# Kernel optimization log

Measured on AMD Instinct MI355X. Metric: run time of the kernel, lower is better.

The kernel has to match this reference:

```python
import jax, jax.numpy as jnp
import numpy as np

N, E = 50000, 1600000
D_IN, D_HID, D_OUT = 256, 256, 128  # 2*output_dim = 256, output_dim = 128


def glorot(key, shape):
    fan_in, fan_out = shape
    limit = np.sqrt(6.0 / (fan_in + fan_out)).astype(np.float32)
    return jax.random.uniform(key, shape, jnp.float32, -limit, limit)


def setup_inputs() -> dict:
    key = jax.random.key(0)
    k0, k1, k2, k3 = jax.random.split(key, 4)
    x = jax.random.normal(k0, (N, D_IN), jnp.float32)
    edge_index = jax.random.randint(k1, (2, E), 0, N, jnp.int32)
    W1 = glorot(k2, (D_IN, D_HID))
    b1 = jnp.zeros((D_HID,), jnp.float32)
    W2 = glorot(k3, (D_HID, D_OUT))
    b2 = jnp.zeros((D_OUT,), jnp.float32)
    return {"x": x, "edge_index": edge_index, "W1": W1, "b1": b1, "W2": W2, "b2": b2}


def gcn_propagate(x, src, dst, num_nodes):
    """One hop of D^-1/2 (A + I) D^-1/2 @ x (PyG gcn_norm with self-loops)."""
    loops = jnp.arange(num_nodes, dtype=src.dtype)
    src_sl = jnp.concatenate([src, loops])  # [E + N]
    dst_sl = jnp.concatenate([dst, loops])
    ones = jnp.ones(src_sl.shape, x.dtype)
    deg = jax.ops.segment_sum(ones, dst_sl, num_segments=num_nodes)  # >= 1 (self-loop)
    dinv = jax.lax.rsqrt(jnp.maximum(deg, 1e-12))
    norm = dinv[src_sl] * dinv[dst_sl]  # [E + N]
    msgs = x[src_sl] * norm[:, None]    # gather + scale, [E+N, D]
    return jax.ops.segment_sum(msgs, dst_sl, num_segments=num_nodes)


def reference(x, edge_index, W1, b1, W2, b2):
    src, dst = edge_index[0], edge_index[1]
    n = x.shape[0]
    # SGConv(K=1): propagate then linear. conv1 + ReLU
    h = jax.nn.relu(gcn_propagate(x, src, dst, n) @ W1 + b1)
    # conv2 (GAE branch)
    return gcn_propagate(h, src, dst, n) @ W2 + b2
```

## Files before the change

### kernel.cpp

```cpp
#include <hip/hip_runtime.h>

typedef short s16x8 __attribute__((ext_vector_type(8)));
typedef float f32x4 __attribute__((ext_vector_type(4)));
typedef float f32x2 __attribute__((ext_vector_type(2)));

#define TILE 2048

__device__ __forceinline__ unsigned int brne(float f) {
    unsigned int u = __float_as_uint(f);
    return (u + 0x7FFFu + ((u >> 16) & 1u)) >> 16;
}
__device__ __forceinline__ float blo(unsigned int u) { return __uint_as_float(u << 16); }
__device__ __forceinline__ float bhi(unsigned int u) { return __uint_as_float(u & 0xFFFF0000u); }

__device__ __forceinline__ void acc8(float* a, const uint4 u, const float wt) {
    a[0] += blo(u.x) * wt; a[1] += bhi(u.x) * wt;
    a[2] += blo(u.y) * wt; a[3] += bhi(u.y) * wt;
    a[4] += blo(u.z) * wt; a[5] += bhi(u.z) * wt;
    a[6] += blo(u.w) * wt; a[7] += bhi(u.w) * wt;
}

__device__ __forceinline__ unsigned int enc_fp8(float v) {
    return __builtin_amdgcn_cvt_pk_fp8_f32(v, v, 0, false) & 0xFF;
}
__device__ __forceinline__ void acc16p(f32x2* a, const uint4 u, const f32x2 w2) {
    a[0] += __builtin_amdgcn_cvt_pk_f32_fp8((int)u.x, false) * w2;
    a[1] += __builtin_amdgcn_cvt_pk_f32_fp8((int)u.x, true)  * w2;
    a[2] += __builtin_amdgcn_cvt_pk_f32_fp8((int)u.y, false) * w2;
    a[3] += __builtin_amdgcn_cvt_pk_f32_fp8((int)u.y, true)  * w2;
    a[4] += __builtin_amdgcn_cvt_pk_f32_fp8((int)u.z, false) * w2;
    a[5] += __builtin_amdgcn_cvt_pk_f32_fp8((int)u.z, true)  * w2;
    a[6] += __builtin_amdgcn_cvt_pk_f32_fp8((int)u.w, false) * w2;
    a[7] += __builtin_amdgcn_cvt_pk_f32_fp8((int)u.w, true)  * w2;
}


__global__ void k_bhist(const int* __restrict__ dst, int* __restrict__ bucket_cnt,
                        int e, int nb) {
    __shared__ int h[256];
    const int tid = threadIdx.x;
    h[tid] = 0;
    __syncthreads();
    const int base = blockIdx.x * TILE + tid;
#pragma unroll
    for (int k = 0; k < 8; k++) {
        const int i = base + k * 256;
        if (i < e) atomicAdd(&h[dst[i] >> 8], 1);
    }
    __syncthreads();
    if (tid < nb && h[tid]) atomicAdd(&bucket_cnt[tid], h[tid]);
}

__global__ void k_bscan(const int* __restrict__ bucket_cnt, int* __restrict__ bucket_base,
                        int* __restrict__ bucket_cursor, int nb, int e) {
    __shared__ int sh[256];
    const int tid = threadIdx.x;
    const int v = (tid < nb) ? bucket_cnt[tid] : 0;
    int x = v;
    sh[tid] = x;
    __syncthreads();
    for (int off = 1; off < 256; off <<= 1) {
        const int t = (tid >= off) ? sh[tid - off] : 0;
        __syncthreads();
        if (tid >= off) { x += t; sh[tid] = x; }
        __syncthreads();
    }
    if (tid < nb) { bucket_base[tid] = x - v; bucket_cursor[tid] = x - v; }
    if (tid == 0) bucket_base[nb] = e;
}

__global__ void k_bscatter(const int* __restrict__ src, const int* __restrict__ dst,
                           int* __restrict__ bucket_cursor, uint2* __restrict__ eb, int e) {
    __shared__ int h[256], hbase[256], h2[256];
    const int tid = threadIdx.x;
    h[tid] = 0; h2[tid] = 0;
    __syncthreads();
    const int base = blockIdx.x * TILE + tid;
    int s[8], d[8], b[8];
    bool val[8];
#pragma unroll
    for (int k = 0; k < 8; k++) {
        const int i = base + k * 256;
        val[k] = i < e;
        if (val[k]) {
            s[k] = src[i]; d[k] = dst[i]; b[k] = d[k] >> 8;
            atomicAdd(&h[b[k]], 1);
        }
    }
    __syncthreads();
    if (h[tid]) hbase[tid] = atomicAdd(&bucket_cursor[tid], h[tid]);
    __syncthreads();
#pragma unroll
    for (int k = 0; k < 8; k++) {
        if (val[k]) {
            const int off = atomicAdd(&h2[b[k]], 1);
            eb[hbase[b[k]] + off] = make_uint2((unsigned)s[k], (unsigned)d[k]);
        }
    }
}

__global__ void k_nhist_scan(const uint2* __restrict__ eb, const int* __restrict__ bucket_base,
                             int* __restrict__ rowptr, int* __restrict__ part,
                             float* __restrict__ dinv, int n) {
    __shared__ int c[256], sh[256];
    const int tid = threadIdx.x, b = blockIdx.x;
    c[tid] = 0;
    __syncthreads();
    const int beg = bucket_base[b], end = bucket_base[b + 1];
    for (int i = beg + tid; i < end; i += 256)
        atomicAdd(&c[eb[i].y & 255], 1);
    __syncthreads();
    const int v = c[tid];
    const int node = b * 256 + tid;
    if (node < n) dinv[node] = rsqrtf((float)(v + 1));
    int x = v;
    sh[tid] = x;
    __syncthreads();
    for (int off = 1; off < 256; off <<= 1) {
        const int t = (tid >= off) ? sh[tid - off] : 0;
        __syncthreads();
        if (tid >= off) { x += t; sh[tid] = x; }
        __syncthreads();
    }
    if (node <= n) rowptr[node] = x - v;
    if (tid == 255) part[b] = x;
}

__global__ void k_place(const uint2* __restrict__ eb, const int* __restrict__ bucket_base,
                        int* __restrict__ rowptr, const int* __restrict__ part,
                        int* __restrict__ es, int n, int nb) {
    __shared__ int sh[256], rp[256], offs[256];
    const int tid = threadIdx.x, b = blockIdx.x;
    int x = (tid < nb) ? part[tid] : 0;
    sh[tid] = x;
    __syncthreads();
    for (int off = 1; off < 256; off <<= 1) {
        const int t = (tid >= off) ? sh[tid - off] : 0;
        __syncthreads();
        if (tid >= off) { x += t; sh[tid] = x; }
        __syncthreads();
    }
    const int prefix = (b > 0) ? sh[b - 1] : 0;
    const int node = b * 256 + tid;
    int rg = 0;
    if (node <= n) {
        rg = rowptr[node] + prefix;
        rowptr[node] = rg;
    }
    rp[tid] = rg;
    offs[tid] = 0;
    __syncthreads();
    const int beg = bucket_base[b], end = bucket_base[b + 1];
    for (int i = beg + tid; i < end; i += 256) {
        const uint2 ed = eb[i];
        const int d = (int)ed.y & 255;
        const int local = atomicAdd(&offs[d], 1);
        es[rp[d] + local] = (int)ed.x;
    }
}

__global__ void k_tW2(const float* __restrict__ W1, const float* __restrict__ W2,
                      unsigned short* __restrict__ W1t, unsigned short* __restrict__ W2t) {
    const int t = blockIdx.x * 256 + threadIdx.x;
    if (t < 65536) {
        const int k = t >> 8, nn = t & 255;
        W1t[nn * 256 + k] = (unsigned short)brne(W1[t]);
    } else {
        const int u = t - 65536;
        const int k = u >> 7, nn = u & 127;
        W2t[nn * 256 + k] = (unsigned short)brne(W2[u]);
    }
}

#define LP 40
template <bool AF32, bool FP8OUT>
__global__ __launch_bounds__(256) void k_gemm(const void* __restrict__ Av,
                                              const unsigned short* __restrict__ Bt,
                                              void* __restrict__ Cout,
                                              int M, int Nc) {
    __shared__ unsigned short As[128 * LP];
    __shared__ unsigned short Bs[128 * LP];

    const int tid = threadIdx.x;
    const int wave = tid >> 6, lane = tid & 63;
    const int wm = (wave >> 1) * 64, wn = (wave & 1) * 64;
    const int l15 = lane & 15, quad = lane >> 4;
    const int mBase = blockIdx.x * 128, nBase = blockIdx.y * 128;

    f32x4 acc[4][4];
#pragma unroll
    for (int i = 0; i < 4; i++)
#pragma unroll
        for (int j = 0; j < 4; j++) acc[i][j] = (f32x4){0.f, 0.f, 0.f, 0.f};

    const int r0 = tid >> 2, kc0 = tid & 3;
    int am0 = mBase + r0;      if (am0 >= M) am0 = M - 1;
    int am1 = mBase + r0 + 64; if (am1 >= M) am1 = M - 1;

    const uint4* Ap0; const uint4* Ap1; const float4* Af0; const float4* Af1;
    if (AF32) {
        Af0 = (const float4*)Av + (size_t)am0 * 64 + kc0 * 2;
        Af1 = (const float4*)Av + (size_t)am1 * 64 + kc0 * 2;
    } else {
        Ap0 = (const uint4*)Av + (size_t)am0 * 32 + kc0;
        Ap1 = (const uint4*)Av + (size_t)am1 * 32 + kc0;
    }
    const uint4* Bp0 = (const uint4*)Bt + (size_t)(nBase + r0) * 32 + kc0;
    const uint4* Bp1 = (const uint4*)Bt + (size_t)(nBase + r0 + 64) * 32 + kc0;

    for (int kt = 0; kt < 8; ++kt) {
        uint4 a0, a1;
        if (AF32) {
            const float4 l0 = Af0[kt * 8], h0 = Af0[kt * 8 + 1];
            const float4 l1 = Af1[kt * 8], h1 = Af1[kt * 8 + 1];
            a0.x = brne(l0.x) | (brne(l0.y) << 16); a0.y = brne(l0.z) | (brne(l0.w) << 16);
            a0.z = brne(h0.x) | (brne(h0.y) << 16); a0.w = brne(h0.z) | (brne(h0.w) << 16);
            a1.x = brne(l1.x) | (brne(l1.y) << 16); a1.y = brne(l1.z) | (brne(l1.w) << 16);
            a1.z = brne(h1.x) | (brne(h1.y) << 16); a1.w = brne(h1.z) | (brne(h1.w) << 16);
        } else {
            a0 = Ap0[kt * 4];
            a1 = Ap1[kt * 4];
        }
        const uint4 b0 = Bp0[kt * 4];
        const uint4 b1 = Bp1[kt * 4];
        __syncthreads();
        *(uint4*)&As[r0 * LP + kc0 * 8] = a0;
        *(uint4*)&As[(r0 + 64) * LP + kc0 * 8] = a1;
        *(uint4*)&Bs[r0 * LP + kc0 * 8] = b0;
        *(uint4*)&Bs[(r0 + 64) * LP + kc0 * 8] = b1;
        __syncthreads();

        s16x8 af[4], bf[4];
#pragma unroll
        for (int i = 0; i < 4; i++)
            af[i] = *(const s16x8*)&As[(wm + i * 16 + l15) * LP + quad * 8];
#pragma unroll
        for (int j = 0; j < 4; j++)
            bf[j] = *(const s16x8*)&Bs[(wn + j * 16 + l15) * LP + quad * 8];
#pragma unroll
        for (int i = 0; i < 4; i++)
#pragma unroll
            for (int j = 0; j < 4; j++)
                acc[i][j] = __builtin_amdgcn_mfma_f32_16x16x32_bf16(af[i], bf[j], acc[i][j], 0, 0, 0);
    }

#pragma unroll
    for (int i = 0; i < 4; i++) {
        const int rowb = mBase + wm + i * 16 + quad * 4;
#pragma unroll
        for (int r = 0; r < 4; r++) {
            const int row = rowb + r;
            if (row < M) {
#pragma unroll
                for (int j = 0; j < 4; j++) {
                    const int col = nBase + wn + j * 16 + l15;
                    if (FP8OUT)
                        ((unsigned char*)Cout)[(size_t)row * Nc + col] =
                            (unsigned char)enc_fp8(acc[i][j][r]);
                    else
                        ((unsigned short*)Cout)[(size_t)row * Nc + col] =
                            (unsigned short)brne(acc[i][j][r]);
                }
            }
        }
    }
}

__global__ void k_prop256f8(const uint4* __restrict__ X4,
                            const int* __restrict__ rowptr,
                            const int* __restrict__ es,
                            const float* __restrict__ dinv,
                            const float* __restrict__ bias,
                            uint4* __restrict__ Y4, int n) {
    const int wid = (int)((blockIdx.x * blockDim.x + threadIdx.x) >> 6);
    const int lane = threadIdx.x & 63;
    const int quad = lane >> 4, l16 = lane & 15;
    if (wid >= n) return;
    const float dd = dinv[wid];
    f32x2 a[8];
#pragma unroll
    for (int k = 0; k < 8; k++) a[k] = (f32x2){0.f, 0.f};

    const int beg = rowptr[wid], end = rowptr[wid + 1];
    int j = beg + quad;
    int sc0 = 0, sc1 = 0;
    float wc0 = 0.f, wc1 = 0.f;
    if (j < end)     { sc0 = es[j];     wc0 = dinv[sc0] * dd; }
    if (j + 4 < end) { sc1 = es[j + 4]; wc1 = dinv[sc1] * dd; }
    if (quad == 0) {
        const uint4 v = X4[(size_t)wid * 16 + l16];
        acc16p(a, v, (f32x2){dd * dd, dd * dd});
    }
    for (; j + 4 < end; j += 8) {
        const uint4 u0 = X4[(size_t)sc0 * 16 + l16];
        const uint4 u1 = X4[(size_t)sc1 * 16 + l16];
        const int jn0 = j + 8, jn1 = j + 12;
        const int sn0 = es[jn0 < end ? jn0 : end - 1];
        const int sn1 = es[jn1 < end ? jn1 : end - 1];
        const float wn0 = dinv[sn0] * dd, wn1 = dinv[sn1] * dd;
        acc16p(a, u0, (f32x2){wc0, wc0});
        acc16p(a, u1, (f32x2){wc1, wc1});
        sc0 = sn0; sc1 = sn1; wc0 = wn0; wc1 = wn1;
    }
    if (j < end) {
        const uint4 u0 = X4[(size_t)sc0 * 16 + l16];
        acc16p(a, u0, (f32x2){wc0, wc0});
    }
#pragma unroll
    for (int k = 0; k < 8; k++) {
        a[k][0] += __shfl_xor(a[k][0], 16);
        a[k][1] += __shfl_xor(a[k][1], 16);
        a[k][0] += __shfl_xor(a[k][0], 32);
        a[k][1] += __shfl_xor(a[k][1], 32);
    }
    if (quad == 0) {
        const float4* bp = (const float4*)bias + l16 * 4;
#pragma unroll
        for (int q = 0; q < 4; q++) {
            const float4 b = bp[q];
            a[2 * q][0]     = fmaxf(a[2 * q][0] + b.x, 0.f);
            a[2 * q][1]     = fmaxf(a[2 * q][1] + b.y, 0.f);
            a[2 * q + 1][0] = fmaxf(a[2 * q + 1][0] + b.z, 0.f);
            a[2 * q + 1][1] = fmaxf(a[2 * q + 1][1] + b.w, 0.f);
        }
        uint4 p0, p1;
        p0.x = brne(a[0][0]) | (brne(a[0][1]) << 16);
        p0.y = brne(a[1][0]) | (brne(a[1][1]) << 16);
        p0.z = brne(a[2][0]) | (brne(a[2][1]) << 16);
        p0.w = brne(a[3][0]) | (brne(a[3][1]) << 16);
        p1.x = brne(a[4][0]) | (brne(a[4][1]) << 16);
        p1.y = brne(a[5][0]) | (brne(a[5][1]) << 16);
        p1.z = brne(a[6][0]) | (brne(a[6][1]) << 16);
        p1.w = brne(a[7][0]) | (brne(a[7][1]) << 16);
        Y4[(size_t)wid * 32 + l16 * 2] = p0;
        Y4[(size_t)wid * 32 + l16 * 2 + 1] = p1;
    }
}

__global__ void k_prop128b(const uint4* __restrict__ X4,
                           const int* __restrict__ rowptr,
                           const int* __restrict__ es,
                           const float* __restrict__ dinv,
                           const float* __restrict__ bias,
                           float* __restrict__ Yout, int n) {
    const int wid = (int)((blockIdx.x * blockDim.x + threadIdx.x) >> 6);
    const int lane = threadIdx.x & 63;
    const int quad = lane >> 4, l16 = lane & 15;
    if (wid >= n) return;
    const float dd = dinv[wid];
    float a[8];
#pragma unroll
    for (int k = 0; k < 8; k++) a[k] = 0.f;

    const int beg = rowptr[wid], end = rowptr[wid + 1];
    int j = beg + quad;
    int sc0 = 0, sc1 = 0;
    float wc0 = 0.f, wc1 = 0.f;
    if (j < end)     { sc0 = es[j];     wc0 = dinv[sc0] * dd; }
    if (j + 4 < end) { sc1 = es[j + 4]; wc1 = dinv[sc1] * dd; }
    if (quad == 0) {
        const uint4 v = X4[(size_t)wid * 16 + l16];
        acc8(a, v, dd * dd);
    }
    for (; j + 4 < end; j += 8) {
        const uint4 u0 = X4[(size_t)sc0 * 16 + l16];
        const uint4 u1 = X4[(size_t)sc1 * 16 + l16];
        const int jn0 = j + 8, jn1 = j + 12;
        const int sn0 = es[jn0 < end ? jn0 : end - 1];
        const int sn1 = es[jn1 < end ? jn1 : end - 1];
        const float wn0 = dinv[sn0] * dd, wn1 = dinv[sn1] * dd;
        acc8(a, u0, wc0);
        acc8(a, u1, wc1);
        sc0 = sn0; sc1 = sn1; wc0 = wn0; wc1 = wn1;
    }
    if (j < end) {
        const uint4 u0 = X4[(size_t)sc0 * 16 + l16];
        acc8(a, u0, wc0);
    }
#pragma unroll
    for (int k = 0; k < 8; k++) {
        a[k] += __shfl_xor(a[k], 16);
        a[k] += __shfl_xor(a[k], 32);
    }
    if (quad == 0) {
        const float4 b0 = ((const float4*)bias)[l16 * 2];
        const float4 b1 = ((const float4*)bias)[l16 * 2 + 1];
        float4* op = (float4*)Yout + (size_t)wid * 32 + l16 * 2;
        op[0] = make_float4(a[0] + b0.x, a[1] + b0.y, a[2] + b0.z, a[3] + b0.w);
        op[1] = make_float4(a[4] + b1.x, a[5] + b1.y, a[6] + b1.z, a[7] + b1.w);
    }
}

extern "C" void kernel_launch(void* const* d_in, const int* in_sizes, int n_in,
                              void* d_out, int out_size, void* d_ws, size_t ws_size,
                              hipStream_t stream) {
    const float* x  = (const float*)d_in[0];
    const int*   ei = (const int*)d_in[1];
    const float* W1 = (const float*)d_in[2];
    const float* b1 = (const float*)d_in[3];
    const float* W2 = (const float*)d_in[4];
    const float* b2 = (const float*)d_in[5];
    float* out = (float*)d_out;

    const int n = in_sizes[0] / 256;
    const int e = in_sizes[1] / 2;
    const int* src = ei;
    const int* dst = ei + e;
    const int nb = (n + 255) >> 8;

    char* wsp = (char*)d_ws;
    size_t off = 0;
    auto alloc = [&](size_t bytes) -> char* {
        char* p = wsp + off;
        off += (bytes + 511) & ~(size_t)511;
        return p;
    };
    float* dinv    = (float*)alloc(sizeof(float) * n);
    int*   rowptr  = (int*)alloc(sizeof(int) * (n + 1));
    int*   part    = (int*)alloc(sizeof(int) * 256);
    int*   bcnt    = (int*)alloc(sizeof(int) * 256);
    int*   bbase   = (int*)alloc(sizeof(int) * 257);
    int*   bcur    = (int*)alloc(sizeof(int) * 256);
    int*   es      = (int*)alloc(sizeof(int) * e);
    unsigned short* W1t = (unsigned short*)alloc(2ull * 256 * 256);
    unsigned short* W2t = (unsigned short*)alloc(2ull * 128 * 256);
    unsigned char*  T1  = (unsigned char*)alloc((size_t)n * 256);
    unsigned short* H   = (unsigned short*)alloc(2ull * n * 256);
    unsigned short* T2  = (unsigned short*)alloc(2ull * n * 128);
    uint2* eb = (uint2*)H;

    const int nb_t = (e + TILE - 1) / TILE;

    (void)hipMemsetAsync(bcnt, 0, sizeof(int) * 256, stream);
    k_bhist<<<nb_t, 256, 0, stream>>>(dst, bcnt, e, nb);
    k_bscan<<<1, 256, 0, stream>>>(bcnt, bbase, bcur, nb, e);
    k_bscatter<<<nb_t, 256, 0, stream>>>(src, dst, bcur, eb, e);
    k_nhist_scan<<<nb, 256, 0, stream>>>(eb, bbase, rowptr, part, dinv, n);
    k_place<<<nb, 256, 0, stream>>>(eb, bbase, rowptr, part, es, n, nb);

    k_tW2<<<(65536 + 32768) / 256, 256, 0, stream>>>(W1, W2, W1t, W2t);

    dim3 g1((n + 127) / 128, 2);
    k_gemm<true, true><<<g1, 256, 0, stream>>>(x, W1t, T1, n, 256);
    k_prop256f8<<<(n + 3) / 4, 256, 0, stream>>>((const uint4*)T1, rowptr, es,
                                                 dinv, b1, (uint4*)H, n);

    dim3 g2((n + 127) / 128, 1);
    k_gemm<false, false><<<g2, 256, 0, stream>>>(H, W2t, T2, n, 128);
    k_prop128b<<<(n + 3) / 4, 256, 0, stream>>>((const uint4*)T2, rowptr, es,
                                                dinv, b2, out, n);
}
```

Baseline: 320.7 us.

## Precompute edge weights in CSR, fuse weight transpose, deepen gather pipeline, packed converts

Several changes land together. The CSR placement kernel can now store (src, weight) pairs with the per-edge normalisation precomputed, so the propagation kernels no longer do a dependent dinv gather per edge. The propagation loops now keep four edges in flight instead of two, using predicated zero-weight tail edges. Separately, the weight transpose is folded into the histogram launch, and bf16/fp8 conversions use packed hardware convert instructions, including paired row stores in the GEMM epilogue. Storing 8-byte edge records doubles the edge-list traffic, and the paired-weight path is only taken when the workspace is large enough.

```diff
diff --git a/kernel.cpp b/kernel.cpp
--- a/kernel.cpp
+++ b/kernel.cpp
@@ -13,16 +13,19 @@
 __device__ __forceinline__ float blo(unsigned int u) { return __uint_as_float(u << 16); }
 __device__ __forceinline__ float bhi(unsigned int u) { return __uint_as_float(u & 0xFFFF0000u); }
 
-__device__ __forceinline__ void acc8(float* a, const uint4 u, const float wt) {
-    a[0] += blo(u.x) * wt; a[1] += bhi(u.x) * wt;
-    a[2] += blo(u.y) * wt; a[3] += bhi(u.y) * wt;
-    a[4] += blo(u.z) * wt; a[5] += bhi(u.z) * wt;
-    a[6] += blo(u.w) * wt; a[7] += bhi(u.w) * wt;
-}
-
-__device__ __forceinline__ unsigned int enc_fp8(float v) {
-    return __builtin_amdgcn_cvt_pk_fp8_f32(v, v, 0, false) & 0xFF;
-}
+__device__ __forceinline__ unsigned int pk_bf16(float lo, float hi) {
+    unsigned int r;
+    asm("v_cvt_pk_bf16_f32 %0, %1, %2" : "=v"(r) : "v"(lo), "v"(hi));
+    return r;
+}
+
+__device__ __forceinline__ void acc8p(f32x2* a, const uint4 u, const f32x2 w2) {
+    a[0] += (f32x2){blo(u.x), bhi(u.x)} * w2;
+    a[1] += (f32x2){blo(u.y), bhi(u.y)} * w2;
+    a[2] += (f32x2){blo(u.z), bhi(u.z)} * w2;
+    a[3] += (f32x2){blo(u.w), bhi(u.w)} * w2;
+}
+
 __device__ __forceinline__ void acc16p(f32x2* a, const uint4 u, const f32x2 w2) {
     a[0] += __builtin_amdgcn_cvt_pk_f32_fp8((int)u.x, false) * w2;
     a[1] += __builtin_amdgcn_cvt_pk_f32_fp8((int)u.x, true)  * w2;
@@ -35,10 +38,24 @@
 }
 
 
-__global__ void k_bhist(const int* __restrict__ dst, int* __restrict__ bucket_cnt,
-                        int e, int nb) {
+__global__ void k_bhist_tw(const int* __restrict__ dst, int* __restrict__ bucket_cnt,
+                           int e, int nb, int nbt,
+                           const float* __restrict__ W1, const float* __restrict__ W2,
+                           unsigned short* __restrict__ W1t, unsigned short* __restrict__ W2t) {
+    const int tid = threadIdx.x;
+    if ((int)blockIdx.x >= nbt) {
+        const int t = ((int)blockIdx.x - nbt) * 256 + tid;
+        if (t < 65536) {
+            const int k = t >> 8, nn = t & 255;
+            W1t[nn * 256 + k] = (unsigned short)brne(W1[t]);
+        } else {
+            const int u = t - 65536;
+            const int k = u >> 7, nn = u & 127;
+            W2t[nn * 256 + k] = (unsigned short)brne(W2[u]);
+        }
+        return;
+    }
     __shared__ int h[256];
-    const int tid = threadIdx.x;
     h[tid] = 0;
     __syncthreads();
     const int base = blockIdx.x * TILE + tid;
@@ -126,10 +143,13 @@
     if (tid == 255) part[b] = x;
 }
 
+template <bool PREW>
 __global__ void k_place(const uint2* __restrict__ eb, const int* __restrict__ bucket_base,
                         int* __restrict__ rowptr, const int* __restrict__ part,
-                        int* __restrict__ es, int n, int nb) {
+                        void* __restrict__ esv, const float* __restrict__ dinv,
+                        int n, int nb) {
     __shared__ int sh[256], rp[256], offs[256];
+    __shared__ float sdv[256];
     const int tid = threadIdx.x, b = blockIdx.x;
     int x = (tid < nb) ? part[tid] : 0;
     sh[tid] = x;
@@ -149,26 +169,26 @@
     }
     rp[tid] = rg;
     offs[tid] = 0;
+    if (PREW) sdv[tid] = (node < n) ? dinv[node] : 0.f;
     __syncthreads();
     const int beg = bucket_base[b], end = bucket_base[b + 1];
-    for (int i = beg + tid; i < end; i += 256) {
-        const uint2 ed = eb[i];
-        const int d = (int)ed.y & 255;
-        const int local = atomicAdd(&offs[d], 1);
-        es[rp[d] + local] = (int)ed.x;
-    }
-}
-
-__global__ void k_tW2(const float* __restrict__ W1, const float* __restrict__ W2,
-                      unsigned short* __restrict__ W1t, unsigned short* __restrict__ W2t) {
-    const int t = blockIdx.x * 256 + threadIdx.x;
-    if (t < 65536) {
-        const int k = t >> 8, nn = t & 255;
-        W1t[nn * 256 + k] = (unsigned short)brne(W1[t]);
+    if (PREW) {
+        int2* es2 = (int2*)esv;
+        for (int i = beg + tid; i < end; i += 256) {
+            const uint2 ed = eb[i];
+            const int sI = (int)ed.x, d = (int)ed.y & 255;
+            const float w = dinv[sI] * sdv[d];
+            const int local = atomicAdd(&offs[d], 1);
+            es2[rp[d] + local] = make_int2(sI, __float_as_int(w));
+        }
     } else {
-        const int u = t - 65536;
-        const int k = u >> 7, nn = u & 127;
-        W2t[nn * 256 + k] = (unsigned short)brne(W2[u]);
+        int* es1 = (int*)esv;
+        for (int i = beg + tid; i < end; i += 256) {
+            const uint2 ed = eb[i];
+            const int d = (int)ed.y & 255;
+            const int local = atomicAdd(&offs[d], 1);
+            es1[rp[d] + local] = (int)ed.x;
+        }
     }
 }
 
@@ -213,10 +233,10 @@
         if (AF32) {
             const float4 l0 = Af0[kt * 8], h0 = Af0[kt * 8 + 1];
             const float4 l1 = Af1[kt * 8], h1 = Af1[kt * 8 + 1];
-            a0.x = brne(l0.x) | (brne(l0.y) << 16); a0.y = brne(l0.z) | (brne(l0.w) << 16);
-            a0.z = brne(h0.x) | (brne(h0.y) << 16); a0.w = brne(h0.z) | (brne(h0.w) << 16);
-            a1.x = brne(l1.x) | (brne(l1.y) << 16); a1.y = brne(l1.z) | (brne(l1.w) << 16);
-            a1.z = brne(h1.x) | (brne(h1.y) << 16); a1.w = brne(h1.z) | (brne(h1.w) << 16);
+            a0.x = pk_bf16(l0.x, l0.y); a0.y = pk_bf16(l0.z, l0.w);
+            a0.z = pk_bf16(h0.x, h0.y); a0.w = pk_bf16(h0.z, h0.w);
+            a1.x = pk_bf16(l1.x, l1.y); a1.y = pk_bf16(l1.z, l1.w);
+            a1.z = pk_bf16(h1.x, h1.y); a1.w = pk_bf16(h1.z, h1.w);
         } else {
             a0 = Ap0[kt * 4];
             a1 = Ap1[kt * 4];
@@ -248,27 +268,38 @@
     for (int i = 0; i < 4; i++) {
         const int rowb = mBase + wm + i * 16 + quad * 4;
 #pragma unroll
-        for (int r = 0; r < 4; r++) {
-            const int row = rowb + r;
-            if (row < M) {
-#pragma unroll
-                for (int j = 0; j < 4; j++) {
-                    const int col = nBase + wn + j * 16 + l15;
-                    if (FP8OUT)
-                        ((unsigned char*)Cout)[(size_t)row * Nc + col] =
-                            (unsigned char)enc_fp8(acc[i][j][r]);
-                    else
-                        ((unsigned short*)Cout)[(size_t)row * Nc + col] =
-                            (unsigned short)brne(acc[i][j][r]);
+        for (int j = 0; j < 4; j++) {
+            const int col = nBase + wn + j * 16 + l15;
+#pragma unroll
+            for (int r = 0; r < 4; r += 2) {
+                if (FP8OUT) {
+                    const unsigned int pk = __builtin_amdgcn_cvt_pk_fp8_f32(
+                        acc[i][j][r], acc[i][j][r + 1], 0, false);
+                    if (rowb + r < M)
+                        ((unsigned char*)Cout)[(size_t)(rowb + r) * Nc + col] =
+                            (unsigned char)pk;
+                    if (rowb + r + 1 < M)
+                        ((unsigned char*)Cout)[(size_t)(rowb + r + 1) * Nc + col] =
+                            (unsigned char)(pk >> 8);
+                } else {
+                    const unsigned int pk = pk_bf16(acc[i][j][r], acc[i][j][r + 1]);
+                    if (rowb + r < M)
+                        ((unsigned short*)Cout)[(size_t)(rowb + r) * Nc + col] =
+                            (unsigned short)pk;
+                    if (rowb + r + 1 < M)
+                        ((unsigned short*)Cout)[(size_t)(rowb + r + 1) * Nc + col] =
+                            (unsigned short)(pk >> 16);
                 }
             }
         }
     }
 }
 
+
+template <bool PREW>
 __global__ void k_prop256f8(const uint4* __restrict__ X4,
                             const int* __restrict__ rowptr,
-                            const int* __restrict__ es,
+                            const void* __restrict__ esv,
                             const float* __restrict__ dinv,
                             const float* __restrict__ bias,
                             uint4* __restrict__ Y4, int n) {
@@ -277,34 +308,60 @@
     const int quad = lane >> 4, l16 = lane & 15;
     if (wid >= n) return;
     const float dd = dinv[wid];
+    const int2* es2 = (const int2*)esv;
+    const int*  es1 = (const int*)esv;
     f32x2 a[8];
 #pragma unroll
     for (int k = 0; k < 8; k++) a[k] = (f32x2){0.f, 0.f};
 
     const int beg = rowptr[wid], end = rowptr[wid + 1];
     int j = beg + quad;
-    int sc0 = 0, sc1 = 0;
-    float wc0 = 0.f, wc1 = 0.f;
-    if (j < end)     { sc0 = es[j];     wc0 = dinv[sc0] * dd; }
-    if (j + 4 < end) { sc1 = es[j + 4]; wc1 = dinv[sc1] * dd; }
+
+    auto EDGE = [&](int jj, int& s, float& w) {
+        const bool v = jj < end;
+        const int idx = v ? jj : 0;
+        if (PREW) {
+            const int2 p = es2[idx];
+            s = p.x;
+            w = v ? __int_as_float(p.y) : 0.f;
+        } else {
+            s = es1[idx];
+            w = v ? dinv[s] * dd : 0.f;
+        }
+    };
+
+    int s0, s1, s2, s3;
+    float w0, w1, w2, w3;
+    EDGE(j, s0, w0); EDGE(j + 4, s1, w1); EDGE(j + 8, s2, w2); EDGE(j + 12, s3, w3);
+
     if (quad == 0) {
         const uint4 v = X4[(size_t)wid * 16 + l16];
         acc16p(a, v, (f32x2){dd * dd, dd * dd});
     }
-    for (; j + 4 < end; j += 8) {
-        const uint4 u0 = X4[(size_t)sc0 * 16 + l16];
-        const uint4 u1 = X4[(size_t)sc1 * 16 + l16];
-        const int jn0 = j + 8, jn1 = j + 12;
-        const int sn0 = es[jn0 < end ? jn0 : end - 1];
-        const int sn1 = es[jn1 < end ? jn1 : end - 1];
-        const float wn0 = dinv[sn0] * dd, wn1 = dinv[sn1] * dd;
-        acc16p(a, u0, (f32x2){wc0, wc0});
-        acc16p(a, u1, (f32x2){wc1, wc1});
-        sc0 = sn0; sc1 = sn1; wc0 = wn0; wc1 = wn1;
-    }
-    if (j < end) {
-        const uint4 u0 = X4[(size_t)sc0 * 16 + l16];
-        acc16p(a, u0, (f32x2){wc0, wc0});
+
+    while (j + 12 < end) {
+        const uint4 u0 = X4[(size_t)s0 * 16 + l16];
+        const uint4 u1 = X4[(size_t)s1 * 16 + l16];
+        const uint4 u2 = X4[(size_t)s2 * 16 + l16];
+        const uint4 u3 = X4[(size_t)s3 * 16 + l16];
+        j += 16;
+        int t0, t1, t2, t3;
+        float x0, x1, x2, x3;
+        EDGE(j, t0, x0); EDGE(j + 4, t1, x1); EDGE(j + 8, t2, x2); EDGE(j + 12, t3, x3);
+        acc16p(a, u0, (f32x2){w0, w0});
+        acc16p(a, u1, (f32x2){w1, w1});
+        acc16p(a, u2, (f32x2){w2, w2});
+        acc16p(a, u3, (f32x2){w3, w3});
+        s0 = t0; s1 = t1; s2 = t2; s3 = t3;
+        w0 = x0; w1 = x1; w2 = x2; w3 = x3;
+    }
+    {
+        const uint4 u0 = X4[(size_t)s0 * 16 + l16];
+        const uint4 u1 = X4[(size_t)s1 * 16 + l16];
+        const uint4 u2 = X4[(size_t)s2 * 16 + l16];
+        acc16p(a, u0, (f32x2){w0, w0});
+        acc16p(a, u1, (f32x2){w1, w1});
+        acc16p(a, u2, (f32x2){w2, w2});
     }
 #pragma unroll
     for (int k = 0; k < 8; k++) {
@@ -324,22 +381,23 @@
             a[2 * q + 1][1] = fmaxf(a[2 * q + 1][1] + b.w, 0.f);
         }
         uint4 p0, p1;
-        p0.x = brne(a[0][0]) | (brne(a[0][1]) << 16);
-        p0.y = brne(a[1][0]) | (brne(a[1][1]) << 16);
-        p0.z = brne(a[2][0]) | (brne(a[2][1]) << 16);
-        p0.w = brne(a[3][0]) | (brne(a[3][1]) << 16);
-        p1.x = brne(a[4][0]) | (brne(a[4][1]) << 16);
-        p1.y = brne(a[5][0]) | (brne(a[5][1]) << 16);
-        p1.z = brne(a[6][0]) | (brne(a[6][1]) << 16);
-        p1.w = brne(a[7][0]) | (brne(a[7][1]) << 16);
+        p0.x = pk_bf16(a[0][0], a[0][1]);
+        p0.y = pk_bf16(a[1][0], a[1][1]);
+        p0.z = pk_bf16(a[2][0], a[2][1]);
+        p0.w = pk_bf16(a[3][0], a[3][1]);
+        p1.x = pk_bf16(a[4][0], a[4][1]);
+        p1.y = pk_bf16(a[5][0], a[5][1]);
+        p1.z = pk_bf16(a[6][0], a[6][1]);
+        p1.w = pk_bf16(a[7][0], a[7][1]);
         Y4[(size_t)wid * 32 + l16 * 2] = p0;
         Y4[(size_t)wid * 32 + l16 * 2 + 1] = p1;
     }
 }
 
+template <bool PREW>
 __global__ void k_prop128b(const uint4* __restrict__ X4,
                            const int* __restrict__ rowptr,
-                           const int* __restrict__ es,
+                           const void* __restrict__ esv,
                            const float* __restrict__ dinv,
                            const float* __restrict__ bias,
                            float* __restrict__ Yout, int n) {
@@ -348,46 +406,74 @@
     const int quad = lane >> 4, l16 = lane & 15;
     if (wid >= n) return;
     const float dd = dinv[wid];
-    float a[8];
-#pragma unroll
-    for (int k = 0; k < 8; k++) a[k] = 0.f;
+    const int2* es2 = (const int2*)esv;
+    const int*  es1 = (const int*)esv;
+    f32x2 a[4];
+#pragma unroll
+    for (int k = 0; k < 4; k++) a[k] = (f32x2){0.f, 0.f};
 
     const int beg = rowptr[wid], end = rowptr[wid + 1];
     int j = beg + quad;
-    int sc0 = 0, sc1 = 0;
-    float wc0 = 0.f, wc1 = 0.f;
-    if (j < end)     { sc0 = es[j];     wc0 = dinv[sc0] * dd; }
-    if (j + 4 < end) { sc1 = es[j + 4]; wc1 = dinv[sc1] * dd; }
+
+    auto EDGE = [&](int jj, int& s, float& w) {
+        const bool v = jj < end;
+        const int idx = v ? jj : 0;
+        if (PREW) {
+            const int2 p = es2[idx];
+            s = p.x;
+            w = v ? __int_as_float(p.y) : 0.f;
+        } else {
+            s = es1[idx];
+            w = v ? dinv[s] * dd : 0.f;
+        }
+    };
+
+    int s0, s1, s2, s3;
+    float w0, w1, w2, w3;
+    EDGE(j, s0, w0); EDGE(j + 4, s1, w1); EDGE(j + 8, s2, w2); EDGE(j + 12, s3, w3);
+
     if (quad == 0) {
         const uint4 v = X4[(size_t)wid * 16 + l16];
-        acc8(a, v, dd * dd);
-    }
-    for (; j + 4 < end; j += 8) {
-        const uint4 u0 = X4[(size_t)sc0 * 16 + l16];
-        const uint4 u1 = X4[(size_t)sc1 * 16 + l16];
-        const int jn0 = j + 8, jn1 = j + 12;
-        const int sn0 = es[jn0 < end ? jn0 : end - 1];
-        const int sn1 = es[jn1 < end ? jn1 : end - 1];
-        const float wn0 = dinv[sn0] * dd, wn1 = dinv[sn1] * dd;
-        acc8(a, u0, wc0);
-        acc8(a, u1, wc1);
-        sc0 = sn0; sc1 = sn1; wc0 = wn0; wc1 = wn1;
-    }
-    if (j < end) {
-        const uint4 u0 = X4[(size_t)sc0 * 16 + l16];
-        acc8(a, u0, wc0);
-    }
-#pragma unroll
-    for (int k = 0; k < 8; k++) {
-        a[k] += __shfl_xor(a[k], 16);
-        a[k] += __shfl_xor(a[k], 32);
+        acc8p(a, v, (f32x2){dd * dd, dd * dd});
+    }
+
+    while (j + 12 < end) {
+        const uint4 u0 = X4[(size_t)s0 * 16 + l16];
+        const uint4 u1 = X4[(size_t)s1 * 16 + l16];
+        const uint4 u2 = X4[(size_t)s2 * 16 + l16];
+        const uint4 u3 = X4[(size_t)s3 * 16 + l16];
+        j += 16;
+        int t0, t1, t2, t3;
+        float x0, x1, x2, x3;
+        EDGE(j, t0, x0); EDGE(j + 4, t1, x1); EDGE(j + 8, t2, x2); EDGE(j + 12, t3, x3);
+        acc8p(a, u0, (f32x2){w0, w0});
+        acc8p(a, u1, (f32x2){w1, w1});
+        acc8p(a, u2, (f32x2){w2, w2});
+        acc8p(a, u3, (f32x2){w3, w3});
+        s0 = t0; s1 = t1; s2 = t2; s3 = t3;
+        w0 = x0; w1 = x1; w2 = x2; w3 = x3;
+    }
+    {
+        const uint4 u0 = X4[(size_t)s0 * 16 + l16];
+        const uint4 u1 = X4[(size_t)s1 * 16 + l16];
+        const uint4 u2 = X4[(size_t)s2 * 16 + l16];
+        acc8p(a, u0, (f32x2){w0, w0});
+        acc8p(a, u1, (f32x2){w1, w1});
+        acc8p(a, u2, (f32x2){w2, w2});
+    }
+#pragma unroll
+    for (int k = 0; k < 4; k++) {
+        a[k][0] += __shfl_xor(a[k][0], 16);
+        a[k][1] += __shfl_xor(a[k][1], 16);
+        a[k][0] += __shfl_xor(a[k][0], 32);
+        a[k][1] += __shfl_xor(a[k][1], 32);
     }
     if (quad == 0) {
         const float4 b0 = ((const float4*)bias)[l16 * 2];
         const float4 b1 = ((const float4*)bias)[l16 * 2 + 1];
         float4* op = (float4*)Yout + (size_t)wid * 32 + l16 * 2;
-        op[0] = make_float4(a[0] + b0.x, a[1] + b0.y, a[2] + b0.z, a[3] + b0.w);
-        op[1] = make_float4(a[4] + b1.x, a[5] + b1.y, a[6] + b1.z, a[7] + b1.w);
+        op[0] = make_float4(a[0][0] + b0.x, a[0][1] + b0.y, a[1][0] + b0.z, a[1][1] + b0.w);
+        op[1] = make_float4(a[2][0] + b1.x, a[2][1] + b1.y, a[3][0] + b1.z, a[3][1] + b1.w);
     }
 }
 
@@ -408,6 +494,13 @@
     const int* dst = ei + e;
     const int nb = (n + 255) >> 8;
 
+    auto al = [](size_t v) { return (v + 511) & ~(size_t)511; };
+    const size_t fixed = al(sizeof(float) * n) + al(sizeof(int) * (n + 1)) +
+                         al(1024) + al(1024) + al(sizeof(int) * 257) + al(1024) +
+                         al(2ull * 256 * 256) + al(2ull * 128 * 256) +
+                         al((size_t)n * 256) + al(2ull * n * 256) + al(2ull * n * 128);
+    const bool prew = (fixed + al(8ull * (size_t)e)) <= ws_size;
+
     char* wsp = (char*)d_ws;
     size_t off = 0;
     auto alloc = [&](size_t bytes) -> char* {
@@ -417,11 +510,11 @@
     };
     float* dinv    = (float*)alloc(sizeof(float) * n);
     int*   rowptr  = (int*)alloc(sizeof(int) * (n + 1));
-    int*   part    = (int*)alloc(sizeof(int) * 256);
-    int*   bcnt    = (int*)alloc(sizeof(int) * 256);
+    int*   part    = (int*)alloc(1024);
+    int*   bcnt    = (int*)alloc(1024);
     int*   bbase   = (int*)alloc(sizeof(int) * 257);
-    int*   bcur    = (int*)alloc(sizeof(int) * 256);
-    int*   es      = (int*)alloc(sizeof(int) * e);
+    int*   bcur    = (int*)alloc(1024);
+    void*  es      = (void*)alloc((prew ? 8ull : 4ull) * (size_t)e);
     unsigned short* W1t = (unsigned short*)alloc(2ull * 256 * 256);
     unsigned short* W2t = (unsigned short*)alloc(2ull * 128 * 256);
     unsigned char*  T1  = (unsigned char*)alloc((size_t)n * 256);
@@ -430,23 +523,33 @@
     uint2* eb = (uint2*)H;
 
     const int nb_t = (e + TILE - 1) / TILE;
+    const int tw_b = (65536 + 32768) / 256;
 
     (void)hipMemsetAsync(bcnt, 0, sizeof(int) * 256, stream);
-    k_bhist<<<nb_t, 256, 0, stream>>>(dst, bcnt, e, nb);
+    k_bhist_tw<<<nb_t + tw_b, 256, 0, stream>>>(dst, bcnt, e, nb, nb_t, W1, W2, W1t, W2t);
     k_bscan<<<1, 256, 0, stream>>>(bcnt, bbase, bcur, nb, e);
     k_bscatter<<<nb_t, 256, 0, stream>>>(src, dst, bcur, eb, e);
     k_nhist_scan<<<nb, 256, 0, stream>>>(eb, bbase, rowptr, part, dinv, n);
-    k_place<<<nb, 256, 0, stream>>>(eb, bbase, rowptr, part, es, n, nb);
-
-    k_tW2<<<(65536 + 32768) / 256, 256, 0, stream>>>(W1, W2, W1t, W2t);
+    if (prew)
+        k_place<true><<<nb, 256, 0, stream>>>(eb, bbase, rowptr, part, es, dinv, n, nb);
+    else
+        k_place<false><<<nb, 256, 0, stream>>>(eb, bbase, rowptr, part, es, dinv, n, nb);
 
     dim3 g1((n + 127) / 128, 2);
     k_gemm<true, true><<<g1, 256, 0, stream>>>(x, W1t, T1, n, 256);
-    k_prop256f8<<<(n + 3) / 4, 256, 0, stream>>>((const uint4*)T1, rowptr, es,
-                                                 dinv, b1, (uint4*)H, n);
+    if (prew)
+        k_prop256f8<true><<<(n + 3) / 4, 256, 0, stream>>>((const uint4*)T1, rowptr, es,
+                                                           dinv, b1, (uint4*)H, n);
+    else
+        k_prop256f8<false><<<(n + 3) / 4, 256, 0, stream>>>((const uint4*)T1, rowptr, es,
+                                                            dinv, b1, (uint4*)H, n);
 
     dim3 g2((n + 127) / 128, 1);
     k_gemm<false, false><<<g2, 256, 0, stream>>>(H, W2t, T2, n, 128);
-    k_prop128b<<<(n + 3) / 4, 256, 0, stream>>>((const uint4*)T2, rowptr, es,
-                                                dinv, b2, out, n);
-}
+    if (prew)
+        k_prop128b<true><<<(n + 3) / 4, 256, 0, stream>>>((const uint4*)T2, rowptr, es,
+                                                          dinv, b2, out, n);
+    else
+        k_prop128b<false><<<(n + 3) / 4, 256, 0, stream>>>((const uint4*)T2, rowptr, es,
+                                                           dinv, b2, out, n);
+}
```

Result: no change. 317.1 us (-1.1%).
